# Optimization experiments

Measured on AMD Instinct MI355X. Metric: run time of the kernel, lower is better.

Reference implementation:

```python
import math
import jax, jax.numpy as jnp
import numpy as np

N_HEAD = 16
ROPE_BASE = 10000.0


def _rope_tables(T, half, dtype):
    # build_sin_cos(seq_len, dim=head_dim//2): inv freq of length `half`
    pos = jnp.arange(T, dtype=jnp.float32)[:, None]                      # [T,1]
    inv = jnp.exp(jnp.arange(0, half * 2, 2, dtype=jnp.float32) * (-math.log(ROPE_BASE) / (half * 2)))  # [half]
    ang = pos * inv                                                       # [T,half]
    return jnp.sin(ang).astype(dtype), jnp.cos(ang).astype(dtype)


def setup_inputs() -> dict:
    key = jax.random.key(0)
    k1, k2, k3 = jax.random.split(key, 3)
    B, T, C = 2, 2048, 2048
    x = jax.random.normal(k1, (B, T, C), dtype=jnp.float32)
    w_qkv = jax.random.normal(k2, (3 * C, C), dtype=jnp.float32) * (1.0 / math.sqrt(C))
    w_proj = jax.random.normal(k3, (C, C), dtype=jnp.float32) * (1.0 / math.sqrt(C))
    return {"x": x, "w_qkv": w_qkv, "w_proj": w_proj}


def reference(x, w_qkv, w_proj):
    B, T, C = x.shape
    H = N_HEAD
    D = C // H
    half = D // 2

    qkv = jnp.einsum('btc,fc->btf', x, w_qkv).reshape(B, T, 3, H, D)
    q, k, v = qkv[:, :, 0], qkv[:, :, 1], qkv[:, :, 2]   # [B,T,H,D]

    sin, cos = _rope_tables(T, half, x.dtype)            # [T,half]
    sin = sin[None, :, None, :]                          # [1,T,1,half]
    cos = cos[None, :, None, :]

    def rot(t):
        t1, t2 = t[..., :half], t[..., half:]
        return jnp.concatenate([t1 * cos - t2 * sin, t2 * cos + t1 * sin], axis=-1)

    q, k = rot(q), rot(k)

    scale = 1.0 / math.sqrt(D)
    scores = jnp.einsum('bthd,bshd->bhts', q, k) * scale  # [B,H,T,T]
    causal = jnp.tril(jnp.ones((T, T), dtype=bool))
    scores = jnp.where(causal[None, None], scores, jnp.finfo(scores.dtype).min)
    probs = jax.nn.softmax(scores, axis=-1)
    out = jnp.einsum('bhts,bshd->bhtd', probs, v)         # [B,H,T,D]

    # Faithful to torch: view(B,T,H,D).permute(0,2,1,3).reshape_as(x)
    # flash output is token-major (B,T,H,D); permute gives (B,H,T,D), then flat reshape to (B,T,C).
    out = out.reshape(B, T, C)
    return jnp.einsum('btc,oc->bto', out, w_proj)
```

## Files before the change

### kernel.cpp

```cpp
#include <hip/hip_runtime.h>
#include <math.h>

typedef __attribute__((ext_vector_type(8))) short short8;
typedef __attribute__((ext_vector_type(4))) float f32x4;
typedef __attribute__((ext_vector_type(16))) float f32x16;
typedef __attribute__((ext_vector_type(4))) unsigned short ushort4v;
typedef __attribute__((ext_vector_type(2))) int int2v;

#define AS1 __attribute__((address_space(1)))
#define AS3 __attribute__((address_space(3)))
#define GLOAD16(src, dst) __builtin_amdgcn_global_load_lds((const AS1 void*)(src), (AS3 void*)(dst), 16, 0, 0)
#define VMWAIT(N) asm volatile("s_waitcnt vmcnt(" #N ")" ::: "memory")
#define LGKM0()   asm volatile("s_waitcnt lgkmcnt(0)" ::: "memory")

__device__ __forceinline__ unsigned short f2b(float f) {
    union { float f; unsigned int u; } c; c.f = f;
    return (unsigned short)((c.u + 0x7FFFu + ((c.u >> 16) & 1u)) >> 16);
}
__device__ __forceinline__ float b2f(unsigned short u) {
    union { unsigned int u; float f; } c; c.u = ((unsigned int)u) << 16;
    return c.f;
}
__device__ __forceinline__ int cvt_pk_bf16(float a, float b) {
    int r;
    asm("v_cvt_pk_bf16_f32 %0, %1, %2" : "=v"(r) : "v"(a), "v"(b));
    return r;
}
__device__ __forceinline__ int xcd_swz(int id, int nwg) {
    int q = nwg >> 3, r = nwg & 7, x = id & 7, rest = id >> 3;
    return (x < r ? x * (q + 1) : r * (q + 1) + (x - r) * q) + rest;
}

__global__ void cvt2(const float* __restrict__ a, const float* __restrict__ bsrc,
                     unsigned short* __restrict__ dst, int n4a) {
    int f = blockIdx.x * 256 + threadIdx.x;
    float4 v = (f < n4a) ? ((const float4*)a)[f] : ((const float4*)bsrc)[f - n4a];
    ushort4v o;
    o.x = f2b(v.x); o.y = f2b(v.y); o.z = f2b(v.z); o.w = f2b(v.w);
    ((ushort4v*)dst)[f] = o;
}

__global__ __launch_bounds__(256) void mid_fused(unsigned short* __restrict__ qkv,
                                                 unsigned short* __restrict__ vtg,
                                                 const float* __restrict__ wproj,
                                                 unsigned short* __restrict__ wpb) {
    int bid = blockIdx.x;
    if (bid < 16384) {
        int tid = bid * 256 + threadIdx.x;
        int i = tid & 63;
        int h = (tid >> 6) & 15;
        int t = (tid >> 10) & 2047;
        int b = tid >> 21;
        float inv = __expf((float)i * -0.14391156608f);
        float ang = (float)t * inv;
        float sn = sinf(ang), cs = cosf(ang);
        size_t base0 = ((size_t)(((b << 11) + t) * 3)) << 11;
#pragma unroll
        for (int s = 0; s < 2; ++s) {
            size_t base = base0 + (size_t)s * 2048 + (h << 7);
            float v1 = b2f(qkv[base + i]);
            float v2 = b2f(qkv[base + 64 + i]);
            qkv[base + i]      = f2b(v1 * cs - v2 * sn);
            qkv[base + 64 + i] = f2b(v2 * cs + v1 * sn);
        }
    } else if (bid < 16384 + 4096) {
        int flat = (bid - 16384) * 256 + threadIdx.x;
        int t = flat & 2047;
        int dc = (flat >> 11) & 15;
        int h = (flat >> 15) & 15;
        int b = flat >> 19;
        short8 v = *(const short8*)(qkv + ((size_t)(b * 2048 + t) * 3 + 2) * 2048 + h * 128 + dc * 8);
        size_t base = ((size_t)(b * 16 + h) * 128 + dc * 8) * 2048 + t;
#pragma unroll
        for (int j = 0; j < 8; j++) vtg[base + (size_t)j * 2048] = (unsigned short)v[j];
    } else {
        int f = (bid - 20480) * 256 + threadIdx.x;
#pragma unroll
        for (int r = 0; r < 4; ++r, f += 1024 * 256) {
            float4 v = ((const float4*)wproj)[f];
            ushort4v o;
            o.x = f2b(v.x); o.y = f2b(v.y); o.z = f2b(v.z); o.w = f2b(v.w);
            ((ushort4v*)wpb)[f] = o;
        }
    }
}

template<int OUT_BF16>
__global__ __launch_bounds__(256) void gemm_nt(const unsigned short* __restrict__ A,
                                               const unsigned short* __restrict__ B,
                                               void* __restrict__ Cout,
                                               int N, int K) {
    constexpr int BK = 64;
    __shared__ unsigned short lA[128 * BK];
    __shared__ unsigned short lB[128 * BK];
    int tid = threadIdx.x;
    int lane = tid & 63, w = tid >> 6;
    int wr = w >> 1, wc = w & 1;
    int col = lane & 15, lg = lane >> 4;
    int nwg = gridDim.x * gridDim.y;
    int id = xcd_swz(blockIdx.y * gridDim.x + blockIdx.x, nwg);
    int rowBase = (id / gridDim.x) * 128;
    int colBase = (id % gridDim.x) * 128;
    f32x4 acc[4][4];
#pragma unroll
    for (int m = 0; m < 4; m++)
#pragma unroll
        for (int n = 0; n < 4; n++) acc[m][n] = (f32x4){0.f, 0.f, 0.f, 0.f};

    int rowS[4], scb[4];
#pragma unroll
    for (int it = 0; it < 4; ++it) {
        int d = it * 4096 + tid * 16;
        int row = d >> 7;
        int cb = d & 127;
        rowS[it] = row;
        scb[it] = cb ^ ((row & 7) << 4);
    }

    for (int kk = 0; kk < K; kk += BK) {
        __syncthreads();
#pragma unroll
        for (int it = 0; it < 4; ++it) {
            const char* srcA = (const char*)A + ((size_t)(rowBase + rowS[it]) * K + kk) * 2 + scb[it];
            const char* srcB = (const char*)B + ((size_t)(colBase + rowS[it]) * K + kk) * 2 + scb[it];
            char* dA = (char*)lA + it * 4096 + w * 1024;
            char* dB = (char*)lB + it * 4096 + w * 1024;
            GLOAD16(srcA, dA);
            GLOAD16(srcB, dB);
        }
        __syncthreads();
#pragma unroll
        for (int kc = 0; kc < 2; ++kc) {
            int cbyte = kc * 64 + 16 * lg;
            short8 af[4], bf[4];
#pragma unroll
            for (int m = 0; m < 4; m++) {
                int row = wr * 64 + m * 16 + col;
                af[m] = *(const short8*)((const char*)lA + row * 128 + (cbyte ^ ((row & 7) << 4)));
            }
#pragma unroll
            for (int n = 0; n < 4; n++) {
                int row = wc * 64 + n * 16 + col;
                bf[n] = *(const short8*)((const char*)lB + row * 128 + (cbyte ^ ((row & 7) << 4)));
            }
#pragma unroll
            for (int m = 0; m < 4; m++)
#pragma unroll
                for (int n = 0; n < 4; n++)
                    acc[m][n] = __builtin_amdgcn_mfma_f32_16x16x32_bf16(af[m], bf[n], acc[m][n], 0, 0, 0);
        }
    }
    int rbase = 4 * lg;
#pragma unroll
    for (int m = 0; m < 4; m++)
#pragma unroll
        for (int reg = 0; reg < 4; ++reg) {
            int r = rowBase + wr * 64 + m * 16 + rbase + reg;
#pragma unroll
            for (int n = 0; n < 4; n++) {
                int c = colBase + wc * 64 + n * 16 + col;
                float v = acc[m][n][reg];
                if (OUT_BF16) ((unsigned short*)Cout)[(size_t)r * N + c] = f2b(v);
                else          ((float*)Cout)[(size_t)r * N + c] = v;
            }
        }
}

__global__ __launch_bounds__(256, 2) void attn_fused(const unsigned short* __restrict__ qkv,
                                                     const unsigned short* __restrict__ vtg,
                                                     unsigned short* __restrict__ out) {
    constexpr int T = 2048;
    __shared__ unsigned short Kl[2][64 * 128];
    __shared__ unsigned short Vl[2][128 * 64];
    int tid = threadIdx.x, lane = tid & 63, w = tid >> 6;
    int q = lane & 31, hi = lane >> 5;
    int id = blockIdx.x;
    int bh = id & 31;
    int u = (id >> 5) & 7;
    int qt = (id >> 8) ? (15 - u) : u;
    int b = bh >> 4, h = bh & 15;
    const float sc2 = 0.08838834764831845f * 1.44269504088896340f;

    int qbase = qt * 128;
    int nkv = 2 * qt + 2;
    int tq = qbase + w * 32 + q;

    short8 qf[8];
    {
        const unsigned short* qp = qkv + ((size_t)(b * T + tq) * 3) * 2048 + h * 128;
#pragma unroll
        for (int s = 0; s < 8; s++) qf[s] = *(const short8*)(qp + s * 16 + hi * 8);
    }
    f32x16 O[4];
#pragma unroll
    for (int dt = 0; dt < 4; dt++)
#pragma unroll
        for (int r = 0; r < 16; r++) O[dt][r] = 0.f;
    float m = -1e30f, l = 0.f;

    auto stageK = [&](int t) {
        int kvb = t * 64;
        char* Kb = (char*)&Kl[t & 1][0];
#pragma unroll
        for (int it = 0; it < 4; ++it) {
            int dby = it * 4096 + tid * 16;
            int row = dby >> 8, cb = dby & 255;
            int scb = cb ^ ((row & 7) << 4);
            const char* src = (const char*)qkv + (((size_t)(b * T + kvb + row) * 3 + 1) * 2048 + h * 128) * 2 + scb;
            GLOAD16(src, Kb + it * 4096 + w * 1024);
        }
    };
    auto stageV = [&](int t) {
        int kvb = t * 64;
        char* Vb = (char*)&Vl[t & 1][0];
#pragma unroll
        for (int it = 0; it < 4; ++it) {
            int dby = it * 4096 + tid * 16;
            int d = dby >> 7, cb = dby & 127;
            int scb = cb ^ ((d & 7) << 4);
            const char* src = (const char*)vtg + (((size_t)bh * 128 + d) * 2048 + kvb) * 2 + scb;
            GLOAD16(src, Vb + it * 4096 + w * 1024);
        }
    };

    stageK(0); stageV(0);

    for (int kv = 0; kv < nkv; ++kv) {
        if (kv + 1 < nkv) {
            stageK(kv + 1);
            stageV(kv + 1);
            VMWAIT(8);
        } else {
            VMWAIT(0);
        }
        __builtin_amdgcn_s_barrier();
        int kvbase = kv * 64;
        bool act = kvbase < qbase + (w + 1) * 32;
        const char* Kb = (const char*)&Kl[kv & 1][0];
        const char* Vb = (const char*)&Vl[kv & 1][0];
        if (act) {
            f32x16 p0, p1;
#pragma unroll
            for (int r = 0; r < 16; r++) { p0[r] = 0.f; p1[r] = 0.f; }
            __builtin_amdgcn_s_setprio(1);
#pragma unroll
            for (int s = 0; s < 8; s++) {
                int cb = s * 32 + hi * 16;
                short8 k0 = *(const short8*)(Kb + q * 256 + (cb ^ ((q & 7) << 4)));
                p0 = __builtin_amdgcn_mfma_f32_32x32x16_bf16(k0, qf[s], p0, 0, 0, 0);
                short8 k1 = *(const short8*)(Kb + (32 + q) * 256 + (cb ^ ((q & 7) << 4)));
                p1 = __builtin_amdgcn_mfma_f32_32x32x16_bf16(k1, qf[s], p1, 0, 0, 0);
            }
            __builtin_amdgcn_s_setprio(0);
#pragma unroll
            for (int r = 0; r < 16; r++) { p0[r] *= sc2; p1[r] *= sc2; }
            bool diag = (kvbase + 63 > qbase + w * 32);
            if (diag) {
#pragma unroll
                for (int r = 0; r < 16; r++) {
                    int kg = kvbase + (r & 3) + 8 * (r >> 2) + 4 * hi;
                    if (kg > tq) p0[r] = -3e38f;
                    if (kg + 32 > tq) p1[r] = -3e38f;
                }
            }
            float mx = -3e38f;
#pragma unroll
            for (int r = 0; r < 16; r++) mx = fmaxf(mx, fmaxf(p0[r], p1[r]));
            mx = fmaxf(mx, __shfl_xor(mx, 32));
            if (!__all(mx - m <= 8.0f)) {
                float mn = fmaxf(m, mx);
                float esc = exp2f(m - mn);
                m = mn;
                l *= esc;
#pragma unroll
                for (int dt = 0; dt < 4; dt++)
#pragma unroll
                    for (int r = 0; r < 16; r++) O[dt][r] *= esc;
            }
            float rs = 0.f;
#pragma unroll
            for (int r = 0; r < 16; r++) {
                p0[r] = exp2f(p0[r] - m); rs += p0[r];
                p1[r] = exp2f(p1[r] - m); rs += p1[r];
            }
            rs += __shfl_xor(rs, 32);
            l += rs;
            union Frag { int i[4]; short8 s; } pa[4];
#pragma unroll
            for (int g = 0; g < 4; g++) {
                float e[8];
#pragma unroll
                for (int j = 0; j < 8; j++) e[j] = (g < 2) ? p0[(g & 1) * 8 + j] : p1[(g & 1) * 8 + j];
                int a0 = cvt_pk_bf16(e[0], e[1]);
                int a1 = cvt_pk_bf16(e[2], e[3]);
                int b0 = cvt_pk_bf16(e[4], e[5]);
                int b1 = cvt_pk_bf16(e[6], e[7]);
                int s0 = hi ? a0 : b0; int r0 = __shfl_xor(s0, 32);
                int s1 = hi ? a1 : b1; int r1 = __shfl_xor(s1, 32);
                pa[g].i[0] = hi ? r0 : a0;
                pa[g].i[1] = hi ? r1 : a1;
                pa[g].i[2] = hi ? b0 : r0;
                pa[g].i[3] = hi ? b1 : r1;
            }
            __builtin_amdgcn_s_setprio(1);
#pragma unroll
            for (int dt = 0; dt < 4; dt++) {
                int d = dt * 32 + q;
#pragma unroll
                for (int ks = 0; ks < 4; ks++) {
                    short8 vfr = *(const short8*)(Vb + d * 128 + ((ks * 32 + hi * 16) ^ ((d & 7) << 4)));
                    O[dt] = __builtin_amdgcn_mfma_f32_32x32x16_bf16(vfr, pa[ks].s, O[dt], 0, 0, 0);
                }
            }
            __builtin_amdgcn_s_setprio(0);
        }
        LGKM0();
        __builtin_amdgcn_s_barrier();
    }
    float linv = 1.0f / l;
    size_t obase = ((size_t)bh * T + tq) * 128;
#pragma unroll
    for (int dt = 0; dt < 4; dt++)
#pragma unroll
        for (int g = 0; g < 4; g++) {
            int d0 = dt * 32 + g * 8 + 4 * hi;
            int w0 = cvt_pk_bf16(O[dt][4 * g + 0] * linv, O[dt][4 * g + 1] * linv);
            int w1 = cvt_pk_bf16(O[dt][4 * g + 2] * linv, O[dt][4 * g + 3] * linv);
            int2v o; o[0] = w0; o[1] = w1;
            *(int2v*)(out + obase + d0) = o;
        }
}

extern "C" void kernel_launch(void* const* d_in, const int* in_sizes, int n_in,
                              void* d_out, int out_size, void* d_ws, size_t ws_size,
                              hipStream_t stream) {
    const float* x      = (const float*)d_in[0];
    const float* w_qkv  = (const float*)d_in[1];
    const float* w_proj = (const float*)d_in[2];
    const int B = 2, T = 2048, C = 2048;
    const int M = B * T;
    const int F = 3 * C;

    size_t need = ((size_t)M * C + (size_t)F * C + (size_t)M * F) * 2;
    if (ws_size < need) return;
    unsigned short* rX  = (unsigned short*)d_ws;
    unsigned short* rW  = rX + (size_t)M * C;
    unsigned short* rQ  = rW + (size_t)F * C;
    unsigned short* rVT = rW;
    unsigned short* rWp = rW + (size_t)B * 16 * 128 * T;

    cvt2<<<(M * C + F * C) / 1024, 256, 0, stream>>>(x, w_qkv, rX, (M * C) / 4);
    gemm_nt<1><<<dim3(F / 128, M / 128), 256, 0, stream>>>(rX, rW, (void*)rQ, F, C);
    mid_fused<<<16384 + 4096 + 1024, 256, 0, stream>>>(rQ, rVT, w_proj, rWp);
    attn_fused<<<512, 256, 0, stream>>>(rQ, rVT, rX);
    gemm_nt<0><<<dim3(C / 128, M / 128), 256, 0, stream>>>(rX, rWp, d_out, C, C);
}
```

Before: 284.5 us.

## Pipeline GEMM with 4-stage async LDS buffering and 128x256 tiles

Reworks the bf16 NT GEMM: workgroups become 512 threads (8 waves) each computing a 128x256 tile. A 4-slot ring of LDS buffers at BK=32 is fed by global_load_lds three steps ahead, synchronised with counted vmcnt waits and a single barrier per step, and setprio raises priority around the MFMA block. This overlaps global loads with compute and removes the double __syncthreads per K step. The cost is 96KB of LDS per workgroup and half as many workgroups, which may limit occupancy and load balance across CUs.

```diff
diff --git a/kernel.cpp b/kernel.cpp
--- a/kernel.cpp
+++ b/kernel.cpp
@@ -86,70 +86,77 @@
 }
 
 template<int OUT_BF16>
-__global__ __launch_bounds__(256) void gemm_nt(const unsigned short* __restrict__ A,
-                                               const unsigned short* __restrict__ B,
-                                               void* __restrict__ Cout,
-                                               int N, int K) {
-    constexpr int BK = 64;
-    __shared__ unsigned short lA[128 * BK];
-    __shared__ unsigned short lB[128 * BK];
-    int tid = threadIdx.x;
-    int lane = tid & 63, w = tid >> 6;
-    int wr = w >> 1, wc = w & 1;
+__global__ __launch_bounds__(512, 2) void gemm_nt(const unsigned short* __restrict__ A,
+                                                  const unsigned short* __restrict__ B,
+                                                  void* __restrict__ Cout,
+                                                  int N, int K) {
+    __shared__ __attribute__((aligned(16))) char lds[98304];
+    int tid = threadIdx.x, lane = tid & 63, w = tid >> 6;
     int col = lane & 15, lg = lane >> 4;
-    int nwg = gridDim.x * gridDim.y;
-    int id = xcd_swz(blockIdx.y * gridDim.x + blockIdx.x, nwg);
-    int rowBase = (id / gridDim.x) * 128;
-    int colBase = (id % gridDim.x) * 128;
+    int wr = w >> 2, wc = w & 3;
+    int gx = gridDim.x;
+    int nwg = gx * gridDim.y;
+    int id = xcd_swz(blockIdx.y * gx + blockIdx.x, nwg);
+    int rowBase = (id / gx) * 128;
+    int colBase = (id % gx) * 256;
+    int nkt = K >> 5;
+
     f32x4 acc[4][4];
 #pragma unroll
     for (int m = 0; m < 4; m++)
 #pragma unroll
         for (int n = 0; n < 4; n++) acc[m][n] = (f32x4){0.f, 0.f, 0.f, 0.f};
 
-    int rowS[4], scb[4];
-#pragma unroll
-    for (int it = 0; it < 4; ++it) {
-        int d = it * 4096 + tid * 16;
-        int row = d >> 7;
-        int cb = d & 127;
-        rowS[it] = row;
-        scb[it] = cb ^ ((row & 7) << 4);
+    auto stageA = [&](int t) {
+        char* dst = lds + (t & 3) * 8192 + w * 1024;
+        int u = w * 64 + lane;
+        int row = u >> 2, ch = u & 3;
+        const char* src = (const char*)A + ((size_t)(rowBase + row) * K + t * 32) * 2
+                          + (((ch ^ (row >> 1)) & 3) << 4);
+        GLOAD16(src, dst);
+    };
+    auto stageB = [&](int t) {
+        char* base = lds + 32768 + (t & 3) * 16384;
+#pragma unroll
+        for (int j = 0; j < 2; ++j) {
+            int u = j * 512 + w * 64 + lane;
+            int row = u >> 2, ch = u & 3;
+            const char* src = (const char*)B + ((size_t)(colBase + row) * K + t * 32) * 2
+                              + (((ch ^ (row >> 1)) & 3) << 4);
+            GLOAD16(src, base + j * 8192 + w * 1024);
+        }
+    };
+
+    stageA(0); stageB(0); stageA(1); stageB(1); stageA(2); stageB(2);
+
+    for (int t = 0; t < nkt; ++t) {
+        if (t + 2 < nkt)      VMWAIT(6);
+        else if (t + 1 < nkt) VMWAIT(3);
+        else                  VMWAIT(0);
+        __builtin_amdgcn_s_barrier();
+        if (t + 3 < nkt) { stageA(t + 3); stageB(t + 3); }
+        const char* Ab = lds + (t & 3) * 8192;
+        const char* Bb = lds + 32768 + (t & 3) * 16384;
+        short8 af[4], bf[4];
+#pragma unroll
+        for (int m = 0; m < 4; ++m) {
+            int row = wr * 64 + m * 16 + col;
+            af[m] = *(const short8*)(Ab + row * 64 + (((lg ^ (row >> 1)) & 3) << 4));
+        }
+#pragma unroll
+        for (int n = 0; n < 4; ++n) {
+            int row = wc * 64 + n * 16 + col;
+            bf[n] = *(const short8*)(Bb + row * 64 + (((lg ^ (row >> 1)) & 3) << 4));
+        }
+        __builtin_amdgcn_s_setprio(1);
+#pragma unroll
+        for (int m = 0; m < 4; ++m)
+#pragma unroll
+            for (int n = 0; n < 4; ++n)
+                acc[m][n] = __builtin_amdgcn_mfma_f32_16x16x32_bf16(af[m], bf[n], acc[m][n], 0, 0, 0);
+        __builtin_amdgcn_s_setprio(0);
     }
 
-    for (int kk = 0; kk < K; kk += BK) {
-        __syncthreads();
-#pragma unroll
-        for (int it = 0; it < 4; ++it) {
-            const char* srcA = (const char*)A + ((size_t)(rowBase + rowS[it]) * K + kk) * 2 + scb[it];
-            const char* srcB = (const char*)B + ((size_t)(colBase + rowS[it]) * K + kk) * 2 + scb[it];
-            char* dA = (char*)lA + it * 4096 + w * 1024;
-            char* dB = (char*)lB + it * 4096 + w * 1024;
-            GLOAD16(srcA, dA);
-            GLOAD16(srcB, dB);
-        }
-        __syncthreads();
-#pragma unroll
-        for (int kc = 0; kc < 2; ++kc) {
-            int cbyte = kc * 64 + 16 * lg;
-            short8 af[4], bf[4];
-#pragma unroll
-            for (int m = 0; m < 4; m++) {
-                int row = wr * 64 + m * 16 + col;
-                af[m] = *(const short8*)((const char*)lA + row * 128 + (cbyte ^ ((row & 7) << 4)));
-            }
-#pragma unroll
-            for (int n = 0; n < 4; n++) {
-                int row = wc * 64 + n * 16 + col;
-                bf[n] = *(const short8*)((const char*)lB + row * 128 + (cbyte ^ ((row & 7) << 4)));
-            }
-#pragma unroll
-            for (int m = 0; m < 4; m++)
-#pragma unroll
-                for (int n = 0; n < 4; n++)
-                    acc[m][n] = __builtin_amdgcn_mfma_f32_16x16x32_bf16(af[m], bf[n], acc[m][n], 0, 0, 0);
-        }
-    }
     int rbase = 4 * lg;
 #pragma unroll
     for (int m = 0; m < 4; m++)
@@ -350,8 +357,8 @@
     unsigned short* rWp = rW + (size_t)B * 16 * 128 * T;
 
     cvt2<<<(M * C + F * C) / 1024, 256, 0, stream>>>(x, w_qkv, rX, (M * C) / 4);
-    gemm_nt<1><<<dim3(F / 128, M / 128), 256, 0, stream>>>(rX, rW, (void*)rQ, F, C);
+    gemm_nt<1><<<dim3(F / 256, M / 128), 512, 0, stream>>>(rX, rW, (void*)rQ, F, C);
     mid_fused<<<16384 + 4096 + 1024, 256, 0, stream>>>(rQ, rVT, w_proj, rWp);
     attn_fused<<<512, 256, 0, stream>>>(rQ, rVT, rX);
-    gemm_nt<0><<<dim3(C / 128, M / 128), 256, 0, stream>>>(rX, rWp, d_out, C, C);
-}
+    gemm_nt<0><<<dim3(C / 256, M / 128), 512, 0, stream>>>(rX, rWp, d_out, C, C);
+}
```

Result: faster. 277.9 us (-2.3%).
